# Performance work log

Measured on AMD Instinct MI355X. Metric: run time of the kernel, lower is better.

## Reference

```python
import jax, jax.numpy as jnp
import numpy as np

B, L, D_MODEL = 2, 2048, 1024
D_INNER, D_STATE, DT_RANK, D_CONV = 2048, 16, 64, 4
EPS = 1e-5


def setup_inputs() -> dict:
    key = jax.random.key(0)
    ks = jax.random.split(key, 12)
    s = lambda fan: 1.0 / np.sqrt(fan)
    return {
        "x": jax.random.normal(ks[0], (B, L, D_MODEL), jnp.float32),
        "norm_w": jnp.ones((D_MODEL,), jnp.float32),
        "W_in": jax.random.normal(ks[1], (2 * D_INNER, D_MODEL), jnp.float32) * s(D_MODEL),
        "W_conv": jax.random.normal(ks[2], (D_INNER, D_CONV), jnp.float32) * s(D_CONV),
        "b_conv": jnp.zeros((D_INNER,), jnp.float32),
        "W_xproj": jax.random.normal(ks[3], (DT_RANK + 2 * D_STATE, D_INNER), jnp.float32) * s(D_INNER),
        "W_dt": jax.random.normal(ks[4], (D_INNER, DT_RANK), jnp.float32) * s(DT_RANK),
        "b_dt": jax.random.normal(ks[5], (D_INNER,), jnp.float32) * 0.1,
        # A initialized as log(1..d_state) per channel (standard Mamba S4D-real init)
        "A_log": jnp.log(jnp.broadcast_to(jnp.arange(1, D_STATE + 1, dtype=jnp.float32), (D_INNER, D_STATE))),
        "D": jnp.ones((D_INNER,), jnp.float32),
        "W_out": jax.random.normal(ks[6], (D_MODEL, D_INNER), jnp.float32) * s(D_INNER),
    }


def _mamba_residual(x, norm_w, W_in, W_conv, b_conv, W_xproj, W_dt, b_dt, A_log, D, W_out):
    # RMSNorm
    xn = x * jax.lax.rsqrt(jnp.mean(x * x, axis=-1, keepdims=True) + EPS) * norm_w
    # in_proj -> split into u (ssm branch) and z (gate)
    xz = jnp.einsum("bld,ed->ble", xn, W_in)            # [b, l, 2*d_inner]
    u, z = jnp.split(xz, 2, axis=-1)                     # each [b, l, d_inner]
    # depthwise causal conv1d over time
    u_t = jnp.transpose(u, (0, 2, 1))                    # [b, d_inner, l]
    u_c = jax.lax.conv_general_dilated(
        u_t, W_conv[:, None, :], window_strides=(1,),
        padding=[(D_CONV - 1, 0)], feature_group_count=D_INNER,
        dimension_numbers=("NCH", "OIH", "NCH"))
    u_c = jax.nn.silu(u_c + b_conv[None, :, None])       # [b, d_inner, l]
    u = jnp.transpose(u_c, (0, 2, 1))                    # [b, l, d_inner]
    # x_proj -> (dt, B, C)
    x_dbl = jnp.einsum("bld,ed->ble", u, W_xproj)        # [b, l, dt_rank+2n]
    dt, Bm, Cm = jnp.split(x_dbl, [DT_RANK, DT_RANK + D_STATE], axis=-1)
    dt = jax.nn.softplus(jnp.einsum("blr,dr->bld", dt, W_dt) + b_dt)  # [b, l, d_inner]
    A = -jnp.exp(A_log)                                  # [d_inner, n]

    # selective scan over time
    def step(h, ins):
        dt_t, B_t, C_t, u_t = ins                        # [b,d],[b,n],[b,n],[b,d]
        dA = jnp.exp(dt_t[..., None] * A)                # [b, d, n]
        h = dA * h + (dt_t * u_t)[..., None] * B_t[:, None, :]
        y = jnp.einsum("bdn,bn->bd", h, C_t)
        return h, y

    h0 = jnp.zeros((x.shape[0], D_INNER, D_STATE), x.dtype)
    ins = (jnp.transpose(dt, (1, 0, 2)), jnp.transpose(Bm, (1, 0, 2)),
           jnp.transpose(Cm, (1, 0, 2)), jnp.transpose(u, (1, 0, 2)))
    _, ys = jax.lax.scan(step, h0, ins)                  # [l, b, d_inner]
    y = jnp.transpose(ys, (1, 0, 2)) + u * D             # [b, l, d_inner]
    y = y * jax.nn.silu(z)
    out = jnp.einsum("ble,de->bld", y, W_out)
    return out + x  # residual (block_mode 'residual'/'none')


def reference(x, norm_w, W_in, W_conv, b_conv, W_xproj, W_dt, b_dt, A_log, D, W_out):
    return _mamba_residual(x, norm_w, W_in, W_conv, b_conv, W_xproj, W_dt, b_dt, A_log, D, W_out)
```

## Files before the change

kernel.cpp:

```cpp
#include <hip/hip_runtime.h>

typedef unsigned short u16;
typedef unsigned int u32;
typedef short bf16x8 __attribute__((ext_vector_type(8)));
typedef float f32x4 __attribute__((ext_vector_type(4)));

static constexpr int LS = 2048;
static constexpr int DM = 1024;
static constexpr int DI = 2048;
static constexpr int DSn = 16;
static constexpr int DTRk = 64;
static constexpr int MR = 4096;
static constexpr int NCH = 64;
static constexpr int CL = LS / NCH;
static constexpr float L2E = 1.44269504f;

#define DEV __device__ __forceinline__

DEV u16 f2bf(float f) {
  u32 u = __float_as_uint(f);
  u32 r = (u + 0x7FFF + ((u >> 16) & 1)) >> 16;
  return (u16)r;
}
DEV float bf2f(u16 h) { return __uint_as_float(((u32)h) << 16); }

DEV void gload16(const u16* g, u16* l) {
  __builtin_amdgcn_global_load_lds((const __attribute__((address_space(1))) u32*)g,
                                   (__attribute__((address_space(3))) u32*)l, 16, 0, 0);
}

DEV void bar() { asm volatile("s_barrier" ::: "memory"); }
DEV void wait_lgkm0() {
  asm volatile("s_waitcnt lgkmcnt(0)" ::: "memory");
  __builtin_amdgcn_sched_barrier(0);
}

#define CALC_POWERS(dst, basev)                                              \
  do {                                                                       \
    const float e1_ = (basev);                                               \
    const float e2_ = e1_ * e1_, e3_ = e2_ * e1_, e4_ = e2_ * e2_;           \
    const float e5_ = e4_ * e1_, e6_ = e4_ * e2_, e7_ = e4_ * e3_,           \
                e8_ = e4_ * e4_;                                             \
    dst[0] = e1_; dst[1] = e2_; dst[2] = e3_; dst[3] = e4_;                  \
    dst[4] = e5_; dst[5] = e6_; dst[6] = e7_; dst[7] = e8_;                  \
    dst[8] = e8_ * e1_;  dst[9] = e8_ * e2_;  dst[10] = e8_ * e3_;           \
    dst[11] = e8_ * e4_; dst[12] = e8_ * e5_; dst[13] = e8_ * e6_;           \
    dst[14] = e8_ * e7_; dst[15] = e8_ * e8_;                                \
  } while (0)

__global__ __launch_bounds__(256) void cvt_weights(const float* __restrict__ W_in,
                                                   const float* __restrict__ W_out,
                                                   const float* __restrict__ W_dt,
                                                   const float* __restrict__ W_xp,
                                                   u16* __restrict__ Win_b,
                                                   u16* __restrict__ Wout_b,
                                                   u16* __restrict__ Wdt_b,
                                                   u16* __restrict__ Wxp_b) {
  const int N0 = 4096 * 1024;
  const int N1 = N0 + 1024 * 2048;
  const int N2 = N1 + 2048 * 64;
  const int N3 = N2 + 128 * 2048;
  int i = blockIdx.x * 256 + threadIdx.x;
  const int stride = gridDim.x * 256;
  for (; i < N3; i += stride) {
    if (i < N0) {
      Win_b[i] = f2bf(W_in[i]);
    } else if (i < N1) {
      const int j = i - N0; Wout_b[j] = f2bf(W_out[j]);
    } else if (i < N2) {
      const int j = i - N1; Wdt_b[j] = f2bf(W_dt[j]);
    } else {
      const int j = i - N2; const int r = j >> 11, c = j & 2047;
      Wxp_b[j] = (r < 96) ? f2bf(W_xp[r * 2048 + c]) : (u16)0;
    }
  }
}

__global__ __launch_bounds__(256) void rmsnorm_kernel(const float* __restrict__ x,
                                                      const float* __restrict__ w,
                                                      u16* __restrict__ xn) {
  const int row = blockIdx.x;
  const int tid = threadIdx.x;
  const float4 v = reinterpret_cast<const float4*>(x + (size_t)row * DM)[tid];
  float ss = v.x * v.x + v.y * v.y + v.z * v.z + v.w * v.w;
#pragma unroll
  for (int o = 32; o; o >>= 1) ss += __shfl_xor(ss, o);
  __shared__ float red[4];
  if ((tid & 63) == 0) red[tid >> 6] = ss;
  __syncthreads();
  const float tot = red[0] + red[1] + red[2] + red[3];
  const float scale = rsqrtf(tot * (1.0f / DM) + 1e-5f);
  const float4 wv = reinterpret_cast<const float4*>(w)[tid];
  ushort4 o4;
  o4.x = f2bf(v.x * scale * wv.x);
  o4.y = f2bf(v.y * scale * wv.y);
  o4.z = f2bf(v.z * scale * wv.z);
  o4.w = f2bf(v.w * scale * wv.w);
  *reinterpret_cast<ushort4*>(&xn[(size_t)row * DM + tid * 4]) = o4;
}

DEV void stage_op(const u16* __restrict__ P, int K, int rowbase, int k0,
                  u16* dst, int tid) {
#pragma unroll
  for (int i = 0; i < 4; ++i) {
    const int row = i * 64 + (tid >> 3);
    const int slot = (tid & 7) ^ (row & 7);
    gload16(P + (size_t)(rowbase + row) * K + k0 + slot * 8, dst + i * 4096 + tid * 8);
  }
}

#define LOAD_A(MH) do { \
  _Pragma("unroll") for (int m_ = 0; m_ < 4; ++m_) \
  _Pragma("unroll") for (int kk_ = 0; kk_ < 2; ++kk_) \
    a[m_][kk_] = *reinterpret_cast<const bf16x8*>( \
        &Asl[curo + wr * 8192 + ((MH) * 64 + m_ * 16 + lrow) * 64 + ((kk_ * 4 + kq) ^ rsw) * 8]); \
} while (0)

#define LOAD_B(NH) do { \
  _Pragma("unroll") for (int n_ = 0; n_ < 2; ++n_) \
  _Pragma("unroll") for (int kk_ = 0; kk_ < 2; ++kk_) \
    b[(NH) * 2 + n_][kk_] = *reinterpret_cast<const bf16x8*>( \
        &Bsl[curo + bh * 8192 + (bq * 64 + ((NH) * 2 + n_) * 16 + lrow) * 64 + ((kk_ * 4 + kq) ^ rsw) * 8]); \
} while (0)

#define MMA_QUAD(MH, NH) do { \
  _Pragma("unroll") for (int m_ = 0; m_ < 4; ++m_) \
  _Pragma("unroll") for (int n_ = 0; n_ < 2; ++n_) \
  _Pragma("unroll") for (int kk_ = 0; kk_ < 2; ++kk_) \
    acc[(MH) * 4 + m_][(NH) * 2 + n_] = __builtin_amdgcn_mfma_f32_16x16x32_bf16( \
        a[m_][kk_], b[(NH) * 2 + n_][kk_], acc[(MH) * 4 + m_][(NH) * 2 + n_], 0, 0, 0); \
} while (0)

template <int EPI>
__global__ __launch_bounds__(512, 2) void gemm256(const u16* __restrict__ A,
                                                  const u16* __restrict__ Bw,
                                                  int M, int N, int K, int Klen,
                                                  u16* __restrict__ outB,
                                                  float* __restrict__ outF) {
  __shared__ __align__(16) u16 Asl[2 * 16384];
  __shared__ __align__(16) u16 Bsl[2 * 16384];
  const int tid = threadIdx.x;
  const int lane = tid & 63;
  const int wid = tid >> 6;
  const int wr = wid >> 2;
  const int wc = wid & 3;
  const int lrow = lane & 15;
  const int kq = lane >> 4;
  const int rsw = lane & 7;
  const int bh = wc >> 1, bq = wc & 1;

  const int nwg = gridDim.x * gridDim.y;
  int wg = blockIdx.y * gridDim.x + blockIdx.x;
  wg = (wg & 7) * (nwg >> 3) + (wg >> 3);
  const int bn = (wg % gridDim.x) * 256;
  const int bm = (wg / gridDim.x) * 256;
  const int koff = blockIdx.z * Klen;

  const int nt = Klen >> 6;

  f32x4 acc[8][4] = {};
  bf16x8 a[4][2], b[4][2];

  stage_op(A, K, bm, koff, &Asl[0], tid);
  stage_op(Bw, K, bn, koff, &Bsl[0], tid);
  stage_op(A, K, bm, koff + 64, &Asl[16384], tid);
  stage_op(Bw, K, bn, koff + 64, &Bsl[16384], tid);
  asm volatile("s_waitcnt vmcnt(8)" ::: "memory");
  __builtin_amdgcn_sched_barrier(0);
  bar();

  for (int t = 0; t < nt; ++t) {
    const int curo = (t & 1) * 16384;
    LOAD_A(0); LOAD_B(0);
    bar(); wait_lgkm0();
    __builtin_amdgcn_s_setprio(1); MMA_QUAD(0, 0); __builtin_amdgcn_s_setprio(0);
    bar();
    LOAD_B(1);
    bar(); wait_lgkm0();
    __builtin_amdgcn_s_setprio(1); MMA_QUAD(0, 1); __builtin_amdgcn_s_setprio(0);
    bar();
    LOAD_A(1);
    if (t < nt - 2) stage_op(Bw, K, bn, koff + (t + 2) * 64, &Bsl[curo], tid);
    bar(); wait_lgkm0();
    __builtin_amdgcn_s_setprio(1); MMA_QUAD(1, 0); __builtin_amdgcn_s_setprio(0);
    bar();
    if (t < nt - 2) stage_op(A, K, bm, koff + (t + 2) * 64, &Asl[curo], tid);
    bar();
    __builtin_amdgcn_s_setprio(1); MMA_QUAD(1, 1); __builtin_amdgcn_s_setprio(0);
    if (t == nt - 2) { asm volatile("s_waitcnt vmcnt(0)" ::: "memory"); }
    else if (t < nt - 2) { asm volatile("s_waitcnt vmcnt(8)" ::: "memory"); }
    bar();
  }

  if (EPI == 0) {
#pragma unroll
    for (int m = 0; m < 8; ++m)
#pragma unroll
      for (int n = 0; n < 4; ++n) {
        const int col = bn + wc * 64 + n * 16 + lrow;
#pragma unroll
        for (int rr = 0; rr < 4; ++rr) {
          const int row = bm + wr * 128 + m * 16 + kq * 4 + rr;
          outB[(size_t)row * N + col] = f2bf(acc[m][n][rr]);
        }
      }
  } else {
    float* dstF = outF + (size_t)blockIdx.z * MR * N;
#pragma unroll
    for (int m = 0; m < 8; ++m)
#pragma unroll
      for (int n = 0; n < 4; ++n) {
        const int col = bn + wc * 64 + n * 16 + lrow;
#pragma unroll
        for (int rr = 0; rr < 4; ++rr) {
          const int row = bm + wr * 128 + m * 16 + kq * 4 + rr;
          dstF[(size_t)row * N + col] = acc[m][n][rr];
        }
      }
  }
}

__global__ __launch_bounds__(256) void outproj_reduce4(const float* __restrict__ p,
                                                       const float* __restrict__ x,
                                                       float* __restrict__ out) {
  const int id = blockIdx.x * 256 + threadIdx.x;
  float4 o = reinterpret_cast<const float4*>(x)[id];
#pragma unroll
  for (int s = 0; s < 4; ++s) {
    const float4 a = reinterpret_cast<const float4*>(p + (size_t)s * MR * 1024)[id];
    o.x += a.x; o.y += a.y; o.z += a.z; o.w += a.w;
  }
  reinterpret_cast<float4*>(out)[id] = o;
}

__global__ __launch_bounds__(256) void gemm_dt(const u16* __restrict__ A,
                                               const u16* __restrict__ Bw,
                                               int M, int N, int K,
                                               u16* __restrict__ outB,
                                               const float* __restrict__ aux) {
  __shared__ __align__(16) u16 As[128 * 32];
  __shared__ __align__(16) u16 Bs[128 * 32];
  const int tid = threadIdx.x;
  const int lane = tid & 63;
  const int wid = tid >> 6;
  const int wr = wid >> 1, wc = wid & 1;
  const int nwg = gridDim.x * gridDim.y;
  int wg = blockIdx.y * gridDim.x + blockIdx.x;
  wg = (wg & 7) * (nwg >> 3) + (wg >> 3);
  const int bn = (wg % gridDim.x) * 128;
  const int bm = (wg / gridDim.x) * 128;
  const int r0 = tid >> 2;
  const int c0 = (tid & 3) * 8;
  const int lrow = lane & 15, kq = lane >> 4;

  f32x4 acc[4][4] = {};

  const u16* Ab = A + (size_t)bm * K;
  const u16* Bb = Bw + (size_t)bn * K;

  for (int k0 = 0; k0 < K; k0 += 32) {
    gload16(Ab + (size_t)r0 * K + k0 + c0, &As[r0 * 32 + c0]);
    gload16(Ab + (size_t)(r0 + 64) * K + k0 + c0, &As[(r0 + 64) * 32 + c0]);
    gload16(Bb + (size_t)r0 * K + k0 + c0, &Bs[r0 * 32 + c0]);
    gload16(Bb + (size_t)(r0 + 64) * K + k0 + c0, &Bs[(r0 + 64) * 32 + c0]);
    __syncthreads();
    bf16x8 af[4], bfr[4];
#pragma unroll
    for (int m = 0; m < 4; ++m)
      af[m] = *reinterpret_cast<const bf16x8*>(&As[(wr * 64 + m * 16 + lrow) * 32 + kq * 8]);
#pragma unroll
    for (int n = 0; n < 4; ++n)
      bfr[n] = *reinterpret_cast<const bf16x8*>(&Bs[(wc * 64 + n * 16 + lrow) * 32 + kq * 8]);
#pragma unroll
    for (int m = 0; m < 4; ++m)
#pragma unroll
      for (int n = 0; n < 4; ++n)
        acc[m][n] = __builtin_amdgcn_mfma_f32_16x16x32_bf16(af[m], bfr[n], acc[m][n], 0, 0, 0);
    __syncthreads();
  }

#pragma unroll
  for (int m = 0; m < 4; ++m) {
#pragma unroll
    for (int n = 0; n < 4; ++n) {
      const int col = bn + wc * 64 + n * 16 + lrow;
#pragma unroll
      for (int r = 0; r < 4; ++r) {
        const int row = bm + wr * 64 + m * 16 + kq * 4 + r;
        const float xv = acc[m][n][r] + aux[col];
        const float sp = fmaxf(xv, 0.f) + log1pf(__expf(-fabsf(xv)));
        outB[(size_t)row * N + col] = f2bf(sp);
      }
    }
  }
}

__global__ __launch_bounds__(256) void gemm_xproj_splitk(const u16* __restrict__ A,
                                                         const u16* __restrict__ Bw,
                                                         float* __restrict__ p0,
                                                         float* __restrict__ p1) {
  __shared__ __align__(16) u16 As[128 * 32];
  __shared__ __align__(16) u16 Bs[128 * 32];
  const int tid = threadIdx.x;
  const int lane = tid & 63;
  const int wid = tid >> 6;
  const int wr = wid >> 1, wc = wid & 1;
  const int kp = blockIdx.x;
  const int bm = blockIdx.y * 128;
  const int koff = kp * 256;
  const int r0 = tid >> 2;
  const int c0 = (tid & 3) * 8;
  const int lrow = lane & 15, kq = lane >> 4;

  f32x4 acc[4][4] = {};
  const u16* Ab = A + (size_t)bm * DI + koff;
  const u16* Bb = Bw + koff;

  for (int k0 = 0; k0 < 256; k0 += 32) {
    gload16(Ab + (size_t)r0 * DI + k0 + c0, &As[r0 * 32 + c0]);
    gload16(Ab + (size_t)(r0 + 64) * DI + k0 + c0, &As[(r0 + 64) * 32 + c0]);
    gload16(Bb + (size_t)r0 * DI + k0 + c0, &Bs[r0 * 32 + c0]);
    gload16(Bb + (size_t)(r0 + 64) * DI + k0 + c0, &Bs[(r0 + 64) * 32 + c0]);
    __syncthreads();
    bf16x8 af[4], bfr[4];
#pragma unroll
    for (int m = 0; m < 4; ++m)
      af[m] = *reinterpret_cast<const bf16x8*>(&As[(wr * 64 + m * 16 + lrow) * 32 + kq * 8]);
#pragma unroll
    for (int n = 0; n < 4; ++n)
      bfr[n] = *reinterpret_cast<const bf16x8*>(&Bs[(wc * 64 + n * 16 + lrow) * 32 + kq * 8]);
#pragma unroll
    for (int m = 0; m < 4; ++m)
#pragma unroll
      for (int n = 0; n < 4; ++n)
        acc[m][n] = __builtin_amdgcn_mfma_f32_16x16x32_bf16(af[m], bfr[n], acc[m][n], 0, 0, 0);
    __syncthreads();
  }

  float* dst = (kp < 4 ? p0 : p1) + (size_t)(kp & 3) * MR * 128;
#pragma unroll
  for (int m = 0; m < 4; ++m)
#pragma unroll
    for (int n = 0; n < 4; ++n) {
      const int col = wc * 64 + n * 16 + lrow;
#pragma unroll
      for (int r = 0; r < 4; ++r) {
        const int row = bm + wr * 64 + m * 16 + kq * 4 + r;
        dst[(size_t)row * 128 + col] = acc[m][n][r];
      }
    }
}

__global__ __launch_bounds__(256) void xproj_reduce(const float* __restrict__ p0,
                                                    const float* __restrict__ p1,
                                                    float* __restrict__ xdbl,
                                                    u16* __restrict__ dtr) {
  const int id = blockIdx.x * 256 + threadIdx.x;
  const int row = id >> 7, col = id & 127;
  float s = 0.f;
#pragma unroll
  for (int kp = 0; kp < 4; ++kp) s += p0[(size_t)kp * MR * 128 + id];
#pragma unroll
  for (int kp = 0; kp < 4; ++kp) s += p1[(size_t)kp * MR * 128 + id];
  if (col < 96) xdbl[(size_t)row * 96 + col] = s;
  if (col < 64) dtr[(size_t)row * 64 + col] = f2bf(s);
}

__global__ __launch_bounds__(256) void conv_silu_kernel(const u16* __restrict__ xz,
                                                        const float* __restrict__ Wc,
                                                        const float* __restrict__ bc,
                                                        u16* __restrict__ uc) {
  const int id = blockIdx.x * 256 + threadIdx.x;
  const int d8 = id & (DI / 8 - 1);
  const int t = (id >> 8) & (LS - 1);
  const int b = id >> 19;
  const int d0 = d8 * 8;
  const size_t rowb = (size_t)b * LS;
  bf16x8 r[4];
#pragma unroll
  for (int k = 0; k < 4; ++k) {
    const int tt = t - 3 + k;
    if (tt >= 0)
      r[k] = *reinterpret_cast<const bf16x8*>(&xz[(rowb + tt) * (2 * DI) + d0]);
    else
      r[k] = bf16x8{0, 0, 0, 0, 0, 0, 0, 0};
  }
  const float4 bc0 = *reinterpret_cast<const float4*>(&bc[d0]);
  const float4 bc1 = *reinterpret_cast<const float4*>(&bc[d0 + 4]);
  const float bcv[8] = {bc0.x, bc0.y, bc0.z, bc0.w, bc1.x, bc1.y, bc1.z, bc1.w};
  u16 o[8];
#pragma unroll
  for (int j = 0; j < 8; ++j) {
    const float4 w = *reinterpret_cast<const float4*>(&Wc[(d0 + j) * 4]);
    float s = bcv[j];
    s += bf2f((u16)r[0][j]) * w.x;
    s += bf2f((u16)r[1][j]) * w.y;
    s += bf2f((u16)r[2][j]) * w.z;
    s += bf2f((u16)r[3][j]) * w.w;
    const float sl = s / (1.f + __expf(-s));
    o[j] = f2bf(sl);
  }
  *reinterpret_cast<bf16x8*>(&uc[(rowb + t) * DI + d0]) =
      *reinterpret_cast<const bf16x8*>(o);
}


__global__ __launch_bounds__(128, 4) void scan_phase1(const u16* __restrict__ dtb,
                                                      const float* __restrict__ xdbl,
                                                      const u16* __restrict__ uc,
                                                      const float* __restrict__ Alog,
                                                      float* __restrict__ P,
                                                      float* __restrict__ S) {
  __shared__ __align__(16) u16 s_dt[16 * 128];
  __shared__ __align__(16) u16 s_uc[16 * 128];
  __shared__ __align__(16) float s_b[16 * 16];
  const int tid = threadIdx.x;
  const int blk = blockIdx.x;
  const int d0 = (blk & 15) * 128;
  const int c = (blk >> 4) & (NCH - 1);
  const int b = blk >> 10;
  const int d = d0 + tid;
  const size_t tbase = (size_t)b * LS + c * CL;

  float Av[16];
  bool fastA = true;
#pragma unroll
  for (int j = 0; j < 16; j += 4) {
    const float4 Alv = *reinterpret_cast<const float4*>(&Alog[d * DSn + j]);
    Av[j + 0] = -__expf(Alv.x); Av[j + 1] = -__expf(Alv.y);
    Av[j + 2] = -__expf(Alv.z); Av[j + 3] = -__expf(Alv.w);
  }
#pragma unroll
  for (int j = 0; j < 16; ++j)
    fastA = fastA && (fabsf(Av[j] + (float)(j + 1)) < 1e-3f * (float)(j + 1));

  float h[16];
#pragma unroll
  for (int j = 0; j < 16; ++j) h[j] = 0.f;
  float sdt = 0.f;

  for (int w = 0; w < 2; ++w) {
    const size_t twb = tbase + w * 16;
#pragma unroll
    for (int j = 0; j < 2; ++j) {
      const int k = j * 128 + tid;
      const int row = k >> 4, col = (k & 15) * 8;
      gload16(dtb + (twb + row) * DI + d0 + col, &s_dt[row * 128 + col]);
      gload16(uc + (twb + row) * DI + d0 + col, &s_uc[row * 128 + col]);
    }
    if (tid < 64) {
      gload16((const u16*)(xdbl + (twb + (tid >> 2)) * 96 + DTRk + (tid & 3) * 4),
              (u16*)&s_b[tid * 4]);
    }
    __syncthreads();
    if (fastA) {
      for (int tr = 0; tr < 16; ++tr) {
        const float dtv = bf2f(s_dt[tr * 128 + tid]);
        const float uv = bf2f(s_uc[tr * 128 + tid]);
        const float du = dtv * uv;
        sdt += dtv;
        float dA[16];
        CALC_POWERS(dA, exp2f(-L2E * dtv));
        float Bf[16];
#pragma unroll
        for (int j = 0; j < 16; j += 4) {
          const float4 Bv = *reinterpret_cast<const float4*>(&s_b[tr * 16 + j]);
          Bf[j] = Bv.x; Bf[j + 1] = Bv.y; Bf[j + 2] = Bv.z; Bf[j + 3] = Bv.w;
        }
#pragma unroll
        for (int j = 0; j < 16; ++j) h[j] = dA[j] * h[j] + du * Bf[j];
      }
    } else {
      for (int tr = 0; tr < 16; ++tr) {
        const float dtv = bf2f(s_dt[tr * 128 + tid]);
        const float uv = bf2f(s_uc[tr * 128 + tid]);
        const float du = dtv * uv;
        sdt += dtv;
        float Bf[16];
#pragma unroll
        for (int j = 0; j < 16; j += 4) {
          const float4 Bv = *reinterpret_cast<const float4*>(&s_b[tr * 16 + j]);
          Bf[j] = Bv.x; Bf[j + 1] = Bv.y; Bf[j + 2] = Bv.z; Bf[j + 3] = Bv.w;
        }
#pragma unroll
        for (int j = 0; j < 16; ++j)
          h[j] = exp2f(dtv * Av[j] * L2E) * h[j] + du * Bf[j];
      }
    }
    __syncthreads();
  }

  const size_t oi = (((size_t)b * NCH + c) * DI + d) * DSn;
  float Pw[16];
  if (fastA) {
    CALC_POWERS(Pw, exp2f(-L2E * sdt));
  } else {
#pragma unroll
    for (int j = 0; j < 16; ++j) Pw[j] = exp2f(Av[j] * L2E * sdt);
  }
#pragma unroll
  for (int j = 0; j < 16; j += 4) {
    float4 Sv = {h[j], h[j + 1], h[j + 2], h[j + 3]};
    float4 Pv = {Pw[j], Pw[j + 1], Pw[j + 2], Pw[j + 3]};
    *reinterpret_cast<float4*>(&S[oi + j]) = Sv;
    *reinterpret_cast<float4*>(&P[oi + j]) = Pv;
  }
}

__global__ __launch_bounds__(256) void scan_phase2(const float* __restrict__ P,
                                                   float* __restrict__ S) {
  const int gid = blockIdx.x * 256 + threadIdx.x;
  const int ng = gid & 3;
  const int d = (gid >> 2) & (DI - 1);
  const int b = gid >> 13;
  float4 h = {0.f, 0.f, 0.f, 0.f};
  for (int cc = 0; cc < NCH; ++cc) {
    const size_t oi = (((size_t)b * NCH + cc) * DI + d) * DSn + ng * 4;
    const float4 Pv = *reinterpret_cast<const float4*>(&P[oi]);
    const float4 Sv = *reinterpret_cast<const float4*>(&S[oi]);
    *reinterpret_cast<float4*>(&S[oi]) = h;
    h.x = Sv.x + Pv.x * h.x;
    h.y = Sv.y + Pv.y * h.y;
    h.z = Sv.z + Pv.z * h.z;
    h.w = Sv.w + Pv.w * h.w;
  }
}

__global__ __launch_bounds__(128, 4) void scan_phase3(const u16* __restrict__ dtb,
                                                      const float* __restrict__ xdbl,
                                                      const u16* __restrict__ uc,
                                                      const u16* __restrict__ xz,
                                                      const float* __restrict__ Alog,
                                                      const float* __restrict__ Dp,
                                                      const float* __restrict__ Hin,
                                                      u16* __restrict__ yb) {
  __shared__ __align__(16) u16 s_dt[16 * 128];
  __shared__ __align__(16) u16 s_uc[16 * 128];
  __shared__ __align__(16) u16 s_z[16 * 128];
  __shared__ __align__(16) float s_bc[16 * 32];
  const int tid = threadIdx.x;
  const int blk = blockIdx.x;
  const int d0 = (blk & 15) * 128;
  const int c = (blk >> 4) & (NCH - 1);
  const int b = blk >> 10;
  const int d = d0 + tid;
  const size_t tbase = (size_t)b * LS + c * CL;

  float Av[16];
  bool fastA = true;
#pragma unroll
  for (int j = 0; j < 16; j += 4) {
    const float4 Alv = *reinterpret_cast<const float4*>(&Alog[d * DSn + j]);
    Av[j + 0] = -__expf(Alv.x); Av[j + 1] = -__expf(Alv.y);
    Av[j + 2] = -__expf(Alv.z); Av[j + 3] = -__expf(Alv.w);
  }
#pragma unroll
  for (int j = 0; j < 16; ++j)
    fastA = fastA && (fabsf(Av[j] + (float)(j + 1)) < 1e-3f * (float)(j + 1));

  const float Dd = Dp[d];
  const size_t oi = (((size_t)b * NCH + c) * DI + d) * DSn;
  float h[16];
#pragma unroll
  for (int j = 0; j < 16; j += 4) {
    const float4 hv = *reinterpret_cast<const float4*>(&Hin[oi + j]);
    h[j] = hv.x; h[j + 1] = hv.y; h[j + 2] = hv.z; h[j + 3] = hv.w;
  }

  for (int w = 0; w < 2; ++w) {
    const size_t twb = tbase + w * 16;
#pragma unroll
    for (int j = 0; j < 2; ++j) {
      const int k = j * 128 + tid;
      const int row = k >> 4, col = (k & 15) * 8;
      gload16(dtb + (twb + row) * DI + d0 + col, &s_dt[row * 128 + col]);
      gload16(uc + (twb + row) * DI + d0 + col, &s_uc[row * 128 + col]);
      gload16(xz + (twb + row) * (2 * DI) + DI + d0 + col, &s_z[row * 128 + col]);
    }
    {
      gload16((const u16*)(xdbl + (twb + (tid >> 3)) * 96 + DTRk + (tid & 7) * 4),
              (u16*)&s_bc[tid * 4]);
    }
    __syncthreads();
#define P3_STEP(DA_STMT)                                                        \
    for (int tr = 0; tr < 16; ++tr) {                                           \
      const float dtv = bf2f(s_dt[tr * 128 + tid]);                             \
      const float uv = bf2f(s_uc[tr * 128 + tid]);                              \
      const float du = dtv * uv;                                                \
      float dA[16];                                                             \
      DA_STMT;                                                                  \
      float Bf[16], Cf[16];                                                     \
      _Pragma("unroll")                                                         \
      for (int j = 0; j < 16; j += 4) {                                         \
        const float4 Bv = *reinterpret_cast<const float4*>(&s_bc[tr * 32 + j]); \
        const float4 Cv = *reinterpret_cast<const float4*>(&s_bc[tr * 32 + 16 + j]); \
        Bf[j] = Bv.x; Bf[j + 1] = Bv.y; Bf[j + 2] = Bv.z; Bf[j + 3] = Bv.w;     \
        Cf[j] = Cv.x; Cf[j + 1] = Cv.y; Cf[j + 2] = Cv.z; Cf[j + 3] = Cv.w;     \
      }                                                                         \
      _Pragma("unroll")                                                         \
      for (int j = 0; j < 16; ++j) h[j] = dA[j] * h[j] + du * Bf[j];            \
      float y0 = 0.f, y1 = 0.f, y2 = 0.f, y3 = 0.f;                             \
      _Pragma("unroll")                                                         \
      for (int j = 0; j < 16; j += 4) {                                         \
        y0 += h[j] * Cf[j];                                                     \
        y1 += h[j + 1] * Cf[j + 1];                                             \
        y2 += h[j + 2] * Cf[j + 2];                                             \
        y3 += h[j + 3] * Cf[j + 3];                                             \
      }                                                                         \
      const float y = (y0 + y1) + (y2 + y3) + uv * Dd;                          \
      const float z = bf2f(s_z[tr * 128 + tid]);                                \
      const float sz = z / (1.f + __expf(-z));                                  \
      yb[(twb + tr) * DI + d] = f2bf(y * sz);                                   \
    }
    if (fastA) {
      P3_STEP(CALC_POWERS(dA, exp2f(-L2E * dtv)));
    } else {
      P3_STEP({ _Pragma("unroll") for (int j = 0; j < 16; ++j) dA[j] = exp2f(dtv * Av[j] * L2E); });
    }
#undef P3_STEP
    __syncthreads();
  }
}

extern "C" void kernel_launch(void* const* d_in, const int* in_sizes, int n_in,
                              void* d_out, int out_size, void* d_ws, size_t ws_size,
                              hipStream_t stream) {
  (void)in_sizes; (void)n_in; (void)out_size; (void)ws_size;
  const float* x      = (const float*)d_in[0];
  const float* norm_w = (const float*)d_in[1];
  const float* W_in   = (const float*)d_in[2];
  const float* W_conv = (const float*)d_in[3];
  const float* b_conv = (const float*)d_in[4];
  const float* W_xp   = (const float*)d_in[5];
  const float* W_dt   = (const float*)d_in[6];
  const float* b_dt   = (const float*)d_in[7];
  const float* A_log  = (const float*)d_in[8];
  const float* Dvec   = (const float*)d_in[9];
  const float* W_out  = (const float*)d_in[10];
  float* out = (float*)d_out;

  char* ws = (char*)d_ws;
  size_t off = 0;
  auto alloc = [&](size_t bytes) -> void* {
    void* p = ws + off;
    off += (bytes + 255) & ~(size_t)255;
    return p;
  };
  u16* Win_b  = (u16*)alloc((size_t)4096 * 1024 * 2);
  u16* Wout_b = (u16*)alloc((size_t)1024 * 2048 * 2);
  u16* Wxp_b  = (u16*)alloc((size_t)128 * 2048 * 2);
  u16* Wdt_b  = (u16*)alloc((size_t)2048 * 64 * 2);
  u16* xn_b   = (u16*)alloc((size_t)MR * DM * 2);
  u16* xz_b   = (u16*)alloc((size_t)MR * 2 * DI * 2);
  u16* uc_b   = (u16*)alloc((size_t)MR * DI * 2);
  float* xdbl = (float*)alloc((size_t)MR * 96 * 4);
  u16* dtr_b  = (u16*)alloc((size_t)MR * 64 * 2);
  u16* dtf_b  = (u16*)alloc((size_t)MR * DI * 2);
  u16* y_b    = (u16*)alloc((size_t)MR * DI * 2);
  float* Sbuf = (float*)alloc((size_t)2 * NCH * DI * DSn * 4);
  float* part0 = (float*)Win_b;
  float* part1 = (float*)xn_b;
  float* Pbuf = (float*)y_b;
  float* opart = (float*)xz_b;

  cvt_weights<<<2048, 256, 0, stream>>>(W_in, W_out, W_dt, W_xp,
                                        Win_b, Wout_b, Wdt_b, Wxp_b);

  rmsnorm_kernel<<<MR, 256, 0, stream>>>(x, norm_w, xn_b);

  gemm256<0><<<dim3(16, 16, 1), 512, 0, stream>>>(xn_b, Win_b, MR, 4096, 1024, 1024,
                                                  xz_b, nullptr);
  conv_silu_kernel<<<4096, 256, 0, stream>>>(xz_b, W_conv, b_conv, uc_b);
  gemm_xproj_splitk<<<dim3(8, 32), 256, 0, stream>>>(uc_b, Wxp_b, part0, part1);
  xproj_reduce<<<2048, 256, 0, stream>>>(part0, part1, xdbl, dtr_b);
  gemm_dt<<<dim3(16, 32), 256, 0, stream>>>(dtr_b, Wdt_b, MR, 2048, 64, dtf_b, b_dt);
  scan_phase1<<<2048, 128, 0, stream>>>(dtf_b, xdbl, uc_b, A_log, Pbuf, Sbuf);
  scan_phase2<<<64, 256, 0, stream>>>(Pbuf, Sbuf);
  scan_phase3<<<2048, 128, 0, stream>>>(dtf_b, xdbl, uc_b, xz_b, A_log, Dvec,
                                        Sbuf, y_b);
  gemm256<1><<<dim3(4, 16, 4), 512, 0, stream>>>(y_b, Wout_b, MR, 1024, 2048, 512,
                                                 nullptr, opart);
  outproj_reduce4<<<4096, 256, 0, stream>>>(opart, x, out);
}
```

Baseline: 230.1 us.

## Software-pipeline LDS fragment loads with double-buffered registers in GEMM main loop

Restructures the 256x256 GEMM main loop to unroll by two K-tiles and use ping-pong register fragments (aX/aY, bX/bY), so LDS reads for the next quadrant are issued before the current MFMA quadrant runs. Explicit lgkmcnt waits and most per-quadrant barriers go away, leaving two barriers per K-tile pair, and global staging into the just-consumed LDS buffer is issued right after each barrier. The goal is to hide LDS latency behind MFMA work and cut synchronisation. The cost is more live registers, a full vmcnt(0) wait each half-iteration, and an implicit assumption that nt is even.

```diff
diff --git a/kernel.cpp b/kernel.cpp
--- a/kernel.cpp
+++ b/kernel.cpp
@@ -30,10 +30,6 @@
 }
 
 DEV void bar() { asm volatile("s_barrier" ::: "memory"); }
-DEV void wait_lgkm0() {
-  asm volatile("s_waitcnt lgkmcnt(0)" ::: "memory");
-  __builtin_amdgcn_sched_barrier(0);
-}
 
 #define CALC_POWERS(dst, basev)                                              \
   do {                                                                       \
@@ -109,26 +105,28 @@
   }
 }
 
-#define LOAD_A(MH) do { \
+#define ISS_A(dst, off, MH) do { \
   _Pragma("unroll") for (int m_ = 0; m_ < 4; ++m_) \
   _Pragma("unroll") for (int kk_ = 0; kk_ < 2; ++kk_) \
-    a[m_][kk_] = *reinterpret_cast<const bf16x8*>( \
-        &Asl[curo + wr * 8192 + ((MH) * 64 + m_ * 16 + lrow) * 64 + ((kk_ * 4 + kq) ^ rsw) * 8]); \
+    dst[m_ * 2 + kk_] = *reinterpret_cast<const bf16x8*>( \
+        &Asl[(off) + wr * 8192 + ((MH) * 64 + m_ * 16 + lrow) * 64 + ((kk_ * 4 + kq) ^ rsw) * 8]); \
 } while (0)
 
-#define LOAD_B(NH) do { \
+#define ISS_B(dst, off, NH) do { \
   _Pragma("unroll") for (int n_ = 0; n_ < 2; ++n_) \
   _Pragma("unroll") for (int kk_ = 0; kk_ < 2; ++kk_) \
-    b[(NH) * 2 + n_][kk_] = *reinterpret_cast<const bf16x8*>( \
-        &Bsl[curo + bh * 8192 + (bq * 64 + ((NH) * 2 + n_) * 16 + lrow) * 64 + ((kk_ * 4 + kq) ^ rsw) * 8]); \
+    dst[n_ * 2 + kk_] = *reinterpret_cast<const bf16x8*>( \
+        &Bsl[(off) + bh * 8192 + (bq * 64 + ((NH) * 2 + n_) * 16 + lrow) * 64 + ((kk_ * 4 + kq) ^ rsw) * 8]); \
 } while (0)
 
-#define MMA_QUAD(MH, NH) do { \
+#define MMAQ(areg, breg, MH, NH) do { \
+  __builtin_amdgcn_s_setprio(1); \
   _Pragma("unroll") for (int m_ = 0; m_ < 4; ++m_) \
   _Pragma("unroll") for (int n_ = 0; n_ < 2; ++n_) \
   _Pragma("unroll") for (int kk_ = 0; kk_ < 2; ++kk_) \
     acc[(MH) * 4 + m_][(NH) * 2 + n_] = __builtin_amdgcn_mfma_f32_16x16x32_bf16( \
-        a[m_][kk_], b[(NH) * 2 + n_][kk_], acc[(MH) * 4 + m_][(NH) * 2 + n_], 0, 0, 0); \
+        areg[m_ * 2 + kk_], breg[n_ * 2 + kk_], acc[(MH) * 4 + m_][(NH) * 2 + n_], 0, 0, 0); \
+  __builtin_amdgcn_s_setprio(0); \
 } while (0)
 
 template <int EPI>
@@ -159,37 +157,49 @@
   const int nt = Klen >> 6;
 
   f32x4 acc[8][4] = {};
-  bf16x8 a[4][2], b[4][2];
+  bf16x8 aX[8], aY[8], bX[4], bY[4];
 
   stage_op(A, K, bm, koff, &Asl[0], tid);
   stage_op(Bw, K, bn, koff, &Bsl[0], tid);
   stage_op(A, K, bm, koff + 64, &Asl[16384], tid);
   stage_op(Bw, K, bn, koff + 64, &Bsl[16384], tid);
   asm volatile("s_waitcnt vmcnt(8)" ::: "memory");
-  __builtin_amdgcn_sched_barrier(0);
   bar();
-
-  for (int t = 0; t < nt; ++t) {
-    const int curo = (t & 1) * 16384;
-    LOAD_A(0); LOAD_B(0);
-    bar(); wait_lgkm0();
-    __builtin_amdgcn_s_setprio(1); MMA_QUAD(0, 0); __builtin_amdgcn_s_setprio(0);
+  ISS_A(aX, 0, 0);
+  ISS_B(bX, 0, 0);
+
+  for (int I = 0; I < (nt >> 1); ++I) {
+    const int u = 2 * I;
+    ISS_B(bY, 0, 1);
+    MMAQ(aX, bX, 0, 0);
+    ISS_A(aY, 0, 1);
+    MMAQ(aX, bY, 0, 1);
+    MMAQ(aY, bX, 1, 0);
+    asm volatile("s_waitcnt vmcnt(0)" ::: "memory");
     bar();
-    LOAD_B(1);
-    bar(); wait_lgkm0();
-    __builtin_amdgcn_s_setprio(1); MMA_QUAD(0, 1); __builtin_amdgcn_s_setprio(0);
+    if (u + 2 < nt) {
+      stage_op(A, K, bm, koff + (u + 2) * 64, &Asl[0], tid);
+      stage_op(Bw, K, bn, koff + (u + 2) * 64, &Bsl[0], tid);
+    }
+    ISS_A(aX, 16384, 0);
+    ISS_B(bX, 16384, 0);
+    MMAQ(aY, bY, 1, 1);
+    ISS_B(bY, 16384, 1);
+    MMAQ(aX, bX, 0, 0);
+    ISS_A(aY, 16384, 1);
+    MMAQ(aX, bY, 0, 1);
+    MMAQ(aY, bX, 1, 0);
+    asm volatile("s_waitcnt vmcnt(0)" ::: "memory");
     bar();
-    LOAD_A(1);
-    if (t < nt - 2) stage_op(Bw, K, bn, koff + (t + 2) * 64, &Bsl[curo], tid);
-    bar(); wait_lgkm0();
-    __builtin_amdgcn_s_setprio(1); MMA_QUAD(1, 0); __builtin_amdgcn_s_setprio(0);
-    bar();
-    if (t < nt - 2) stage_op(A, K, bm, koff + (t + 2) * 64, &Asl[curo], tid);
-    bar();
-    __builtin_amdgcn_s_setprio(1); MMA_QUAD(1, 1); __builtin_amdgcn_s_setprio(0);
-    if (t == nt - 2) { asm volatile("s_waitcnt vmcnt(0)" ::: "memory"); }
-    else if (t < nt - 2) { asm volatile("s_waitcnt vmcnt(8)" ::: "memory"); }
-    bar();
+    if (u + 3 < nt) {
+      stage_op(A, K, bm, koff + (u + 3) * 64, &Asl[16384], tid);
+      stage_op(Bw, K, bn, koff + (u + 3) * 64, &Bsl[16384], tid);
+    }
+    if (u + 2 < nt) {
+      ISS_A(aX, 0, 0);
+      ISS_B(bX, 0, 0);
+    }
+    MMAQ(aY, bY, 1, 1);
   }
 
   if (EPI == 0) {
```

Result: slower. 251.1 us (+9.1%).
